# Performance work log

Hardware: AMD Instinct MI355X
Metric: run time of the kernel (lower is better)

Reference implementation:

```python
import jax, jax.numpy as jnp
import numpy as np

D, H, O, E, TOPK = 1024, 4096, 1024, 8, 2
B, L = 2, 2048
ROUTE_SCALE = 1.0


def setup_inputs() -> dict:
    key = jax.random.key(0)
    ks = jax.random.split(key, 7)
    # xavier-uniform bound for gate weight (E, D)
    gb = float(np.sqrt(6.0 / (E + D)))
    return {
        "x": jax.random.normal(ks[0], (B, L, D), dtype=jnp.float32),
        "gate_w": jax.random.uniform(ks[1], (E, D), jnp.float32, -gb, gb),
        "gate_b": jnp.zeros((E,), jnp.float32),
        "w1": jax.random.normal(ks[2], (E, D, H), jnp.float32) * 0.02,
        "b1": jnp.zeros((E, H), jnp.float32),
        "w2": jax.random.normal(ks[3], (E, H, O), jnp.float32) * 0.02,
        "b2": jnp.zeros((E, O), jnp.float32),
    }


def reference(x, gate_w, gate_b, w1, b1, w2, b2):
    Bb, Ll, Dd = x.shape
    N = Bb * Ll
    x_flat = x.reshape(N, Dd)  # (N, D)

    # ---- Gate: softmax router + top-k ----
    logits = x_flat @ gate_w.T + gate_b              # (N, E)
    probs = jax.nn.softmax(logits * ROUTE_SCALE, axis=-1)
    topk_vals, topk_idx = jax.lax.top_k(probs, TOPK)  # (N, K)

    # dense gate: zeros except selected experts keep their prob
    dense_gate = jnp.zeros((N, E), probs.dtype).at[
        jnp.arange(N)[:, None], topk_idx
    ].set(topk_vals)                                  # (N, E)

    # ---- Experts (vectorized over E; gate weights are exactly zero for
    #      non-selected experts, so the combine reproduces the sparse
    #      gather-MLP-scatter math of the original loop) ----
    h = jax.nn.relu(jnp.einsum("nd,edh->neh", x_flat, w1) + b1)  # (N, E, H)
    y = jnp.einsum("neh,eho->neo", h, w2) + b2                   # (N, E, O)
    out_flat = jnp.einsum("ne,neo->no", dense_gate, y)           # (N, O)

    return out_flat.reshape(Bb, Ll, O)
```

## Files before the change

### kernel.cpp

```cpp
#include <hip/hip_runtime.h>
#include <hip/hip_bf16.h>
#include <stdint.h>

#define NTOK 4096
#define DDIM 1024
#define HDIM 4096
#define ODIM 1024
#define NEXP 8
#define BM 128
#define BN 128
#define BK 64
#define CAPROWS (NTOK * 2 + NEXP * BM)
#define MAXTILES (CAPROWS / BM)

typedef float f32x4_t __attribute__((ext_vector_type(4)));
typedef short bf16x8_t __attribute__((ext_vector_type(8)));
using bf16_t = __hip_bfloat16;

__device__ __forceinline__ void gll16(const void* g, void* l) {
  __builtin_amdgcn_global_load_lds(
      (__attribute__((address_space(1))) void*)(void*)g,
      (__attribute__((address_space(3))) void*)l, 16, 0, 0);
}

__global__ __launch_bounds__(256) void gate_kernel(
    const float* __restrict__ x, const float* __restrict__ gw,
    const float* __restrict__ gb, int* __restrict__ top_idx,
    float* __restrict__ top_val, int* __restrict__ counts) {
  int n = blockIdx.x * 4 + (threadIdx.x >> 6);
  int l = threadIdx.x & 63;
  const float4* xv = (const float4*)(x + (size_t)n * DDIM);
  float4 xs[4];
#pragma unroll
  for (int j = 0; j < 4; ++j) xs[j] = xv[l + 64 * j];
  float part[NEXP];
#pragma unroll
  for (int e = 0; e < NEXP; ++e) {
    const float4* wv = (const float4*)(gw + (size_t)e * DDIM);
    float s = 0.f;
#pragma unroll
    for (int j = 0; j < 4; ++j) {
      float4 w4 = wv[l + 64 * j];
      s += xs[j].x * w4.x + xs[j].y * w4.y + xs[j].z * w4.z + xs[j].w * w4.w;
    }
    part[e] = s;
  }
#pragma unroll
  for (int off = 32; off > 0; off >>= 1)
#pragma unroll
    for (int e = 0; e < NEXP; ++e) part[e] += __shfl_xor(part[e], off, 64);

  float m = -1e30f;
#pragma unroll
  for (int e = 0; e < NEXP; ++e) { part[e] += gb[e]; m = fmaxf(m, part[e]); }
  float ssum = 0.f;
#pragma unroll
  for (int e = 0; e < NEXP; ++e) { part[e] = expf(part[e] - m); ssum += part[e]; }
  int i0 = 0; float v0 = part[0];
#pragma unroll
  for (int e = 1; e < NEXP; ++e) if (part[e] > v0) { v0 = part[e]; i0 = e; }
  int i1 = -1; float v1 = -1e30f;
#pragma unroll
  for (int e = 0; e < NEXP; ++e) if (e != i0 && part[e] > v1) { v1 = part[e]; i1 = e; }
  if (l == 0) {
    float inv = 1.f / ssum;
    top_idx[n * 2] = i0; top_idx[n * 2 + 1] = i1;
    top_val[n * 2] = v0 * inv; top_val[n * 2 + 1] = v1 * inv;
    atomicAdd(&counts[i0], 1); atomicAdd(&counts[i1], 1);
  }
}

__global__ void plan_kernel(const int* __restrict__ counts, int* __restrict__ offs,
                            int* __restrict__ tile_e, int* __restrict__ tile_r) {
  if (threadIdx.x != 0 || blockIdx.x != 0) return;
  int off = 0, t = 0;
  for (int e = 0; e < NEXP; ++e) {
    offs[e] = off;
    int padded = ((counts[e] + BM - 1) / BM) * BM;
    for (int r = 0; r < padded; r += BM) { tile_e[t] = e; tile_r[t] = off + r; ++t; }
    off += padded;
  }
  offs[NEXP] = off;
  for (; t < MAXTILES; ++t) { tile_e[t] = -1; tile_r[t] = 0; }
}

__global__ __launch_bounds__(128) void gather_kernel(
    const float* __restrict__ x, const int* __restrict__ top_idx,
    const int* __restrict__ offs, int* __restrict__ cursors,
    int* __restrict__ slot_for, bf16_t* __restrict__ Xg) {
  int a = blockIdx.x;
  __shared__ int s_slot;
  if (threadIdx.x == 0) {
    int e = top_idx[a];
    int pos = atomicAdd(&cursors[e], 1);
    int slot = offs[e] + pos;
    slot_for[a] = slot;
    s_slot = slot;
  }
  __syncthreads();
  int slot = s_slot;
  int n = a >> 1;
  const float4* xv = (const float4*)(x + (size_t)n * DDIM);
  float4 a0 = xv[threadIdx.x * 2], a1 = xv[threadIdx.x * 2 + 1];
  __align__(16) bf16_t tmp[8] = {
      __float2bfloat16(a0.x), __float2bfloat16(a0.y),
      __float2bfloat16(a0.z), __float2bfloat16(a0.w),
      __float2bfloat16(a1.x), __float2bfloat16(a1.y),
      __float2bfloat16(a1.z), __float2bfloat16(a1.w)};
  *(uint4*)(Xg + (size_t)slot * DDIM + threadIdx.x * 8) = *(const uint4*)tmp;
}

__global__ __launch_bounds__(256) void convT_kernel(
    const float* __restrict__ src, bf16_t* __restrict__ dst, int R, int C) {
  __shared__ float tile[64][65];
  int e = blockIdx.z;
  int c0 = blockIdx.x * 64, r0 = blockIdx.y * 64;
  const float* s = src + ((size_t)e * R + r0) * C + c0;
  int tc = threadIdx.x & 63, tr = threadIdx.x >> 6;
#pragma unroll
  for (int p = 0; p < 16; ++p) {
    int r = tr + p * 4;
    tile[r][tc] = s[(size_t)r * C + tc];
  }
  __syncthreads();
  bf16_t* d = dst + ((size_t)e * C + c0) * R + r0;
  int oc = threadIdx.x >> 2;
  int orq = (threadIdx.x & 3) * 16;
#pragma unroll
  for (int j = 0; j < 4; ++j) {
    __align__(8) bf16_t v[4];
#pragma unroll
    for (int i = 0; i < 4; ++i) v[i] = __float2bfloat16(tile[orq + j * 4 + i][oc]);
    *(uint2*)(d + (size_t)oc * R + orq + j * 4) = *(const uint2*)v;
  }
}

template <int KTOT, int NTOT, int WHICH>
__global__ __launch_bounds__(256, 2) void gemm_kernel(
    const bf16_t* __restrict__ A, const bf16_t* __restrict__ Bt,
    const float* __restrict__ bias, void* __restrict__ Cout,
    const int* __restrict__ tile_e, const int* __restrict__ tile_r) {
  int e = tile_e[blockIdx.y];
  if (e < 0) return;
  int row0 = tile_r[blockIdx.y];
  int n0 = blockIdx.x * BN;
  int tid = threadIdx.x;

  __shared__ bf16_t As[2][BM * BK];
  __shared__ bf16_t Bs[2][BN * BK];

  const bf16_t* Ab = A + (size_t)row0 * KTOT;
  const bf16_t* Bb = Bt + ((size_t)e * NTOT + n0) * KTOT;

  int l = tid & 63;
  int w = tid >> 6;
  int wr = (w >> 1) * 64;
  int wc = (w & 1) * 64;
  int lrow = l & 15, lk = l >> 4;

  int st_row = tid >> 3;
  int st_lc = (tid & 7) ^ (st_row & 7);

  int aoff[2][4], boff[2][4];
#pragma unroll
  for (int ks = 0; ks < 2; ++ks) {
    int pc = (ks * 4 + lk) ^ (l & 7);
#pragma unroll
    for (int f = 0; f < 4; ++f) {
      aoff[ks][f] = ((wr + f * 16 + lrow) * BK) * 2 + pc * 16;
      boff[ks][f] = ((wc + f * 16 + lrow) * BK) * 2 + pc * 16;
    }
  }

  f32x4_t acc[4][4];
#pragma unroll
  for (int i = 0; i < 4; ++i)
#pragma unroll
    for (int j = 0; j < 4; ++j) acc[i][j] = (f32x4_t){0.f, 0.f, 0.f, 0.f};

  const int NKT = KTOT / BK;

#pragma unroll
  for (int it = 0; it < 4; ++it) {
    int r = st_row + it * 32;
    gll16(Ab + (size_t)r * KTOT + st_lc * 8, (char*)As[0] + (it * 256 + tid) * 16);
    gll16(Bb + (size_t)r * KTOT + st_lc * 8, (char*)Bs[0] + (it * 256 + tid) * 16);
  }
  __syncthreads();

  int cur = 0;
  for (int kt = 0; kt < NKT; ++kt) {
    if (kt + 1 < NKT) {
      int kb = (kt + 1) * BK + st_lc * 8;
#pragma unroll
      for (int it = 0; it < 4; ++it) {
        int r = st_row + it * 32;
        gll16(Ab + (size_t)r * KTOT + kb, (char*)As[cur ^ 1] + (it * 256 + tid) * 16);
        gll16(Bb + (size_t)r * KTOT + kb, (char*)Bs[cur ^ 1] + (it * 256 + tid) * 16);
      }
    }
#pragma unroll
    for (int ks = 0; ks < 2; ++ks) {
      bf16x8_t av[4], bv[4];
#pragma unroll
      for (int f = 0; f < 4; ++f)
        av[f] = *(const bf16x8_t*)((const char*)As[cur] + aoff[ks][f]);
#pragma unroll
      for (int f = 0; f < 4; ++f)
        bv[f] = *(const bf16x8_t*)((const char*)Bs[cur] + boff[ks][f]);
#pragma unroll
      for (int fm = 0; fm < 4; ++fm)
#pragma unroll
        for (int fn = 0; fn < 4; ++fn)
          acc[fm][fn] = __builtin_amdgcn_mfma_f32_16x16x32_bf16(
              av[fm], bv[fn], acc[fm][fn], 0, 0, 0);
    }
    __syncthreads();
    cur ^= 1;
  }

#pragma unroll
  for (int fn = 0; fn < 4; ++fn) {
    int col = n0 + wc + fn * 16 + lrow;
    float bv = bias[e * NTOT + col];
#pragma unroll
    for (int fm = 0; fm < 4; ++fm) {
      size_t rbase = (size_t)row0 + wr + fm * 16 + lk * 4;
#pragma unroll
      for (int i = 0; i < 4; ++i) {
        float v = acc[fm][fn][i] + bv;
        if (WHICH == 1) {
          v = v > 0.f ? v : 0.f;
          ((bf16_t*)Cout)[(rbase + i) * NTOT + col] = __float2bfloat16(v);
        } else {
          ((float*)Cout)[(rbase + i) * NTOT + col] = v;
        }
      }
    }
  }
}

__global__ __launch_bounds__(256) void combine_kernel(
    const float* __restrict__ Y, const int* __restrict__ slot_for,
    const float* __restrict__ top_val, float* __restrict__ out) {
  int n = blockIdx.x;
  int s0 = slot_for[n * 2], s1 = slot_for[n * 2 + 1];
  float v0 = top_val[n * 2], v1 = top_val[n * 2 + 1];
  int t = threadIdx.x;
  float4 a = ((const float4*)(Y + (size_t)s0 * ODIM))[t];
  float4 b = ((const float4*)(Y + (size_t)s1 * ODIM))[t];
  float4 r;
  r.x = v0 * a.x + v1 * b.x;
  r.y = v0 * a.y + v1 * b.y;
  r.z = v0 * a.z + v1 * b.z;
  r.w = v0 * a.w + v1 * b.w;
  ((float4*)(out + (size_t)n * ODIM))[t] = r;
}

__global__ void zero_meta_kernel(int* p) {
  if (threadIdx.x < 16) p[threadIdx.x] = 0;
}

extern "C" void kernel_launch(void* const* d_in, const int* in_sizes, int n_in,
                              void* d_out, int out_size, void* d_ws, size_t ws_size,
                              hipStream_t stream) {
  const float* x  = (const float*)d_in[0];
  const float* gw = (const float*)d_in[1];
  const float* gb = (const float*)d_in[2];
  const float* w1 = (const float*)d_in[3];
  const float* b1 = (const float*)d_in[4];
  const float* w2 = (const float*)d_in[5];
  const float* b2 = (const float*)d_in[6];
  float* out = (float*)d_out;

  char* ws = (char*)d_ws;
  size_t off = 0;
  auto alloc = [&](size_t bytes) {
    void* p = ws + off;
    off = (off + bytes + 255) & ~(size_t)255;
    return p;
  };
  bf16_t* w1T = (bf16_t*)alloc((size_t)NEXP * HDIM * DDIM * 2);
  bf16_t* w2T = (bf16_t*)alloc((size_t)NEXP * ODIM * HDIM * 2);
  bf16_t* Xg  = (bf16_t*)alloc((size_t)CAPROWS * DDIM * 2);
  bf16_t* Hb  = (bf16_t*)alloc((size_t)CAPROWS * HDIM * 2);
  int* counts  = (int*)alloc(64);
  int* cursors = counts + 8;
  int* offs    = (int*)alloc(64);
  int* tile_e  = (int*)alloc(MAXTILES * 4);
  int* tile_r  = (int*)alloc(MAXTILES * 4);
  int* top_idx = (int*)alloc((size_t)NTOK * 2 * 4);
  float* top_val = (float*)alloc((size_t)NTOK * 2 * 4);
  int* slot_for = (int*)alloc((size_t)NTOK * 2 * 4);
  float* Yb = (float*)w1T;

  hipLaunchKernelGGL(zero_meta_kernel, dim3(1), dim3(64), 0, stream, counts);
  hipMemsetAsync(Xg, 0, (size_t)CAPROWS * DDIM * 2, stream);
  hipLaunchKernelGGL(convT_kernel, dim3(HDIM / 64, DDIM / 64, NEXP), dim3(256), 0,
                     stream, w1, w1T, DDIM, HDIM);
  hipLaunchKernelGGL(convT_kernel, dim3(ODIM / 64, HDIM / 64, NEXP), dim3(256), 0,
                     stream, w2, w2T, HDIM, ODIM);
  hipLaunchKernelGGL(gate_kernel, dim3(NTOK / 4), dim3(256), 0, stream,
                     x, gw, gb, top_idx, top_val, counts);
  hipLaunchKernelGGL(plan_kernel, dim3(1), dim3(1), 0, stream,
                     counts, offs, tile_e, tile_r);
  hipLaunchKernelGGL(gather_kernel, dim3(NTOK * 2), dim3(128), 0, stream,
                     x, top_idx, offs, cursors, slot_for, Xg);
  hipLaunchKernelGGL((gemm_kernel<DDIM, HDIM, 1>), dim3(HDIM / BN, MAXTILES),
                     dim3(256), 0, stream, Xg, w1T, b1, Hb, tile_e, tile_r);
  hipLaunchKernelGGL((gemm_kernel<HDIM, ODIM, 2>), dim3(ODIM / BN, MAXTILES),
                     dim3(256), 0, stream, Hb, w2T, b2, Yb, tile_e, tile_r);
  hipLaunchKernelGGL(combine_kernel, dim3(NTOK), dim3(256), 0, stream,
                     Yb, slot_for, top_val, out);
}
```

Before: 797.9 us.

## Replace expert GEMM with 256x256 8-wave pipelined kernel and XCD-aware tile swizzle

Rewrites the grouped expert GEMM to use 256x256 tiles with 8 waves, splitting the A and B loads into half-tile stages that overlap explicitly with MFMA phases. Explicit barriers, waitcnts and setprio control the schedule, and block ids are remapped so neighbouring tiles land on the same XCD. The transpose-convert kernel also switches to 16-byte stores. The larger tile raises data reuse and arithmetic intensity, but it also increases padding waste per expert (BM capacity grows) and lowers the block count, and it uses 128 KB of LDS per block.

Result: faster. 736.2 us (-7.7%).

```diff
diff --git a/kernel.cpp b/kernel.cpp
--- a/kernel.cpp
+++ b/kernel.cpp
@@ -7,8 +7,8 @@
 #define HDIM 4096
 #define ODIM 1024
 #define NEXP 8
-#define BM 128
-#define BN 128
+#define BM 256
+#define BN 256
 #define BK 64
 #define CAPROWS (NTOK * 2 + NEXP * BM)
 #define MAXTILES (CAPROWS / BM)
@@ -16,6 +16,23 @@
 typedef float f32x4_t __attribute__((ext_vector_type(4)));
 typedef short bf16x8_t __attribute__((ext_vector_type(8)));
 using bf16_t = __hip_bfloat16;
+
+#define S_BARRIER()                         \
+  do {                                      \
+    __builtin_amdgcn_sched_barrier(0);      \
+    __builtin_amdgcn_s_barrier();           \
+    __builtin_amdgcn_sched_barrier(0);      \
+  } while (0)
+#define WAIT_LGKM0()                                  \
+  do {                                                \
+    asm volatile("s_waitcnt lgkmcnt(0)" ::: "memory");\
+    __builtin_amdgcn_sched_barrier(0);                \
+  } while (0)
+#define WAIT_VMCNT(n)                                       \
+  do {                                                      \
+    asm volatile("s_waitcnt vmcnt(" #n ")" ::: "memory");   \
+    __builtin_amdgcn_sched_barrier(0);                      \
+  } while (0)
 
 __device__ __forceinline__ void gll16(const void* g, void* l) {
   __builtin_amdgcn_global_load_lds(
@@ -123,117 +140,164 @@
     tile[r][tc] = s[(size_t)r * C + tc];
   }
   __syncthreads();
-  bf16_t* d = dst + ((size_t)e * C + c0) * R + r0;
-  int oc = threadIdx.x >> 2;
-  int orq = (threadIdx.x & 3) * 16;
-#pragma unroll
-  for (int j = 0; j < 4; ++j) {
-    __align__(8) bf16_t v[4];
-#pragma unroll
-    for (int i = 0; i < 4; ++i) v[i] = __float2bfloat16(tile[orq + j * 4 + i][oc]);
-    *(uint2*)(d + (size_t)oc * R + orq + j * 4) = *(const uint2*)v;
+  bf16_t* dcol = dst + ((size_t)e * C + c0) * R + r0;
+  int t = threadIdx.x;
+#pragma unroll
+  for (int it = 0; it < 2; ++it) {
+    int c = (t >> 3) + it * 32;
+    int r8 = (t & 7) * 8;
+    __align__(16) bf16_t v[8];
+#pragma unroll
+    for (int j = 0; j < 8; ++j) v[j] = __float2bfloat16(tile[r8 + j][c]);
+    *(uint4*)(dcol + (size_t)c * R + r8) = *(const uint4*)v;
   }
 }
 
 template <int KTOT, int NTOT, int WHICH>
-__global__ __launch_bounds__(256, 2) void gemm_kernel(
+__global__ __launch_bounds__(512, 2) void gemm8_kernel(
     const bf16_t* __restrict__ A, const bf16_t* __restrict__ Bt,
     const float* __restrict__ bias, void* __restrict__ Cout,
     const int* __restrict__ tile_e, const int* __restrict__ tile_r) {
-  int e = tile_e[blockIdx.y];
+  constexpr int NCOL = NTOT / BN;
+  int nwg = gridDim.x;
+  int bid = blockIdx.x;
+  int q = nwg >> 3, rr = nwg & 7;
+  int xcd = bid & 7, pos = bid >> 3;
+  int swz = (xcd < rr ? xcd * (q + 1) : rr * (q + 1) + (xcd - rr) * q) + pos;
+  int ty = swz / NCOL, tx = swz % NCOL;
+
+  int e = tile_e[ty];
   if (e < 0) return;
-  int row0 = tile_r[blockIdx.y];
-  int n0 = blockIdx.x * BN;
+  int row0 = tile_r[ty];
+  int n0 = tx * BN;
+
+  __shared__ char smem[131072];
   int tid = threadIdx.x;
-
-  __shared__ bf16_t As[2][BM * BK];
-  __shared__ bf16_t Bs[2][BN * BK];
+  int w = tid >> 6, l = tid & 63;
+  int wm = w >> 2, wn = w & 3;
+  int lrow = l & 15, lk = l >> 4;
 
   const bf16_t* Ab = A + (size_t)row0 * KTOT;
   const bf16_t* Bb = Bt + ((size_t)e * NTOT + n0) * KTOT;
 
-  int l = tid & 63;
-  int w = tid >> 6;
-  int wr = (w >> 1) * 64;
-  int wc = (w & 1) * 64;
-  int lrow = l & 15, lk = l >> 4;
-
-  int st_row = tid >> 3;
-  int st_lc = (tid & 7) ^ (st_row & 7);
-
-  int aoff[2][4], boff[2][4];
-#pragma unroll
-  for (int ks = 0; ks < 2; ++ks) {
-    int pc = (ks * 4 + lk) ^ (l & 7);
-#pragma unroll
-    for (int f = 0; f < 4; ++f) {
-      aoff[ks][f] = ((wr + f * 16 + lrow) * BK) * 2 + pc * 16;
-      boff[ks][f] = ((wc + f * 16 + lrow) * BK) * 2 + pc * 16;
+  int sidx0 = tid, sidx1 = 512 + tid;
+  int sr0 = sidx0 >> 3, sc0 = (sidx0 & 7) ^ (sr0 & 7);
+  int sr1 = sidx1 >> 3, sc1 = (sidx1 & 7) ^ (sr1 & 7);
+
+  auto stageA = [&](int kt, int h, int d) {
+    char* lb = smem + d * 32768 + h * 16384;
+    const bf16_t* g = Ab + (size_t)(h * 128) * KTOT + kt * BK;
+    gll16(g + (size_t)sr0 * KTOT + sc0 * 8, lb + sidx0 * 16);
+    gll16(g + (size_t)sr1 * KTOT + sc1 * 8, lb + sidx1 * 16);
+  };
+  auto stageB = [&](int kt, int h, int d) {
+    char* lb = smem + 65536 + d * 32768 + h * 16384;
+    const bf16_t* g = Bb + (size_t)(h * 128) * KTOT + kt * BK;
+    gll16(g + (size_t)sr0 * KTOT + sc0 * 8, lb + sidx0 * 16);
+    gll16(g + (size_t)sr1 * KTOT + sc1 * 8, lb + sidx1 * 16);
+  };
+
+  int abase = (wm * 128 + lrow) * 128;
+  int bbase = (wn * 64 + lrow) * 128;
+  int p0 = ((lk) ^ (lrow & 7)) * 16;
+  int p1 = ((4 + lk) ^ (lrow & 7)) * 16;
+
+  f32x4_t acc[8][4];
+#pragma unroll
+  for (int m = 0; m < 8; ++m)
+#pragma unroll
+    for (int n = 0; n < 4; ++n) acc[m][n] = (f32x4_t){0.f, 0.f, 0.f, 0.f};
+
+  const int NKT = KTOT / BK;
+
+  stageA(0, 0, 0); stageA(0, 1, 0);
+  stageB(0, 0, 0); stageB(0, 1, 0);
+  stageA(1, 0, 1); stageA(1, 1, 1);
+  WAIT_VMCNT(4);
+  S_BARRIER();
+
+  for (int t = 0; t < NKT; ++t) {
+    int d = t & 1;
+    const char* Ad = smem + d * 32768;
+    const char* Bd = smem + 65536 + d * 32768;
+    bf16x8_t ak0[8], ak1[8], bv[4];
+#pragma unroll
+    for (int m = 0; m < 8; ++m)
+      ak0[m] = *(const bf16x8_t*)(Ad + abase + m * 2048 + p0);
+#pragma unroll
+    for (int n = 0; n < 4; ++n)
+      bv[n] = *(const bf16x8_t*)(Bd + bbase + n * 2048 + p0);
+    if (t + 1 < NKT) stageB(t + 1, 0, d ^ 1);
+    S_BARRIER();
+    WAIT_LGKM0();
+    __builtin_amdgcn_s_setprio(1);
+#pragma unroll
+    for (int m = 0; m < 4; ++m)
+#pragma unroll
+      for (int n = 0; n < 4; ++n)
+        acc[m][n] = __builtin_amdgcn_mfma_f32_16x16x32_bf16(ak0[m], bv[n], acc[m][n], 0, 0, 0);
+    __builtin_amdgcn_s_setprio(0);
+    S_BARRIER();
+#pragma unroll
+    for (int m = 0; m < 8; ++m)
+      ak1[m] = *(const bf16x8_t*)(Ad + abase + m * 2048 + p1);
+    if (t + 1 < NKT) stageB(t + 1, 1, d ^ 1);
+    S_BARRIER();
+    WAIT_LGKM0();
+    __builtin_amdgcn_s_setprio(1);
+#pragma unroll
+    for (int m = 4; m < 8; ++m)
+#pragma unroll
+      for (int n = 0; n < 4; ++n)
+        acc[m][n] = __builtin_amdgcn_mfma_f32_16x16x32_bf16(ak0[m], bv[n], acc[m][n], 0, 0, 0);
+    __builtin_amdgcn_s_setprio(0);
+    S_BARRIER();
+#pragma unroll
+    for (int n = 0; n < 4; ++n)
+      bv[n] = *(const bf16x8_t*)(Bd + bbase + n * 2048 + p1);
+    if (t + 2 < NKT) stageA(t + 2, 0, d);
+    S_BARRIER();
+    WAIT_LGKM0();
+    __builtin_amdgcn_s_setprio(1);
+#pragma unroll
+    for (int m = 0; m < 4; ++m)
+#pragma unroll
+      for (int n = 0; n < 4; ++n)
+        acc[m][n] = __builtin_amdgcn_mfma_f32_16x16x32_bf16(ak1[m], bv[n], acc[m][n], 0, 0, 0);
+    __builtin_amdgcn_s_setprio(0);
+    S_BARRIER();
+    if (t + 2 < NKT) {
+      stageA(t + 2, 1, d);
+      WAIT_VMCNT(4);
+    } else {
+      WAIT_VMCNT(0);
     }
-  }
-
-  f32x4_t acc[4][4];
-#pragma unroll
-  for (int i = 0; i < 4; ++i)
-#pragma unroll
-    for (int j = 0; j < 4; ++j) acc[i][j] = (f32x4_t){0.f, 0.f, 0.f, 0.f};
-
-  const int NKT = KTOT / BK;
-
-#pragma unroll
-  for (int it = 0; it < 4; ++it) {
-    int r = st_row + it * 32;
-    gll16(Ab + (size_t)r * KTOT + st_lc * 8, (char*)As[0] + (it * 256 + tid) * 16);
-    gll16(Bb + (size_t)r * KTOT + st_lc * 8, (char*)Bs[0] + (it * 256 + tid) * 16);
-  }
-  __syncthreads();
-
-  int cur = 0;
-  for (int kt = 0; kt < NKT; ++kt) {
-    if (kt + 1 < NKT) {
-      int kb = (kt + 1) * BK + st_lc * 8;
-#pragma unroll
-      for (int it = 0; it < 4; ++it) {
-        int r = st_row + it * 32;
-        gll16(Ab + (size_t)r * KTOT + kb, (char*)As[cur ^ 1] + (it * 256 + tid) * 16);
-        gll16(Bb + (size_t)r * KTOT + kb, (char*)Bs[cur ^ 1] + (it * 256 + tid) * 16);
-      }
-    }
-#pragma unroll
-    for (int ks = 0; ks < 2; ++ks) {
-      bf16x8_t av[4], bv[4];
-#pragma unroll
-      for (int f = 0; f < 4; ++f)
-        av[f] = *(const bf16x8_t*)((const char*)As[cur] + aoff[ks][f]);
-#pragma unroll
-      for (int f = 0; f < 4; ++f)
-        bv[f] = *(const bf16x8_t*)((const char*)Bs[cur] + boff[ks][f]);
-#pragma unroll
-      for (int fm = 0; fm < 4; ++fm)
-#pragma unroll
-        for (int fn = 0; fn < 4; ++fn)
-          acc[fm][fn] = __builtin_amdgcn_mfma_f32_16x16x32_bf16(
-              av[fm], bv[fn], acc[fm][fn], 0, 0, 0);
-    }
-    __syncthreads();
-    cur ^= 1;
-  }
-
-#pragma unroll
-  for (int fn = 0; fn < 4; ++fn) {
-    int col = n0 + wc + fn * 16 + lrow;
-    float bv = bias[e * NTOT + col];
-#pragma unroll
-    for (int fm = 0; fm < 4; ++fm) {
-      size_t rbase = (size_t)row0 + wr + fm * 16 + lk * 4;
+    S_BARRIER();
+    __builtin_amdgcn_s_setprio(1);
+#pragma unroll
+    for (int m = 4; m < 8; ++m)
+#pragma unroll
+      for (int n = 0; n < 4; ++n)
+        acc[m][n] = __builtin_amdgcn_mfma_f32_16x16x32_bf16(ak1[m], bv[n], acc[m][n], 0, 0, 0);
+    __builtin_amdgcn_s_setprio(0);
+    S_BARRIER();
+  }
+
+#pragma unroll
+  for (int n = 0; n < 4; ++n) {
+    int col = n0 + wn * 64 + n * 16 + lrow;
+    float bb = bias[e * NTOT + col];
+#pragma unroll
+    for (int m = 0; m < 8; ++m) {
+      size_t rb = (size_t)row0 + wm * 128 + m * 16 + lk * 4;
 #pragma unroll
       for (int i = 0; i < 4; ++i) {
-        float v = acc[fm][fn][i] + bv;
+        float v = acc[m][n][i] + bb;
         if (WHICH == 1) {
           v = v > 0.f ? v : 0.f;
-          ((bf16_t*)Cout)[(rbase + i) * NTOT + col] = __float2bfloat16(v);
+          ((bf16_t*)Cout)[(rb + i) * NTOT + col] = __float2bfloat16(v);
         } else {
-          ((float*)Cout)[(rbase + i) * NTOT + col] = v;
+          ((float*)Cout)[(rb + i) * NTOT + col] = v;
         }
       }
     }
@@ -306,10 +370,12 @@
                      counts, offs, tile_e, tile_r);
   hipLaunchKernelGGL(gather_kernel, dim3(NTOK * 2), dim3(128), 0, stream,
                      x, top_idx, offs, cursors, slot_for, Xg);
-  hipLaunchKernelGGL((gemm_kernel<DDIM, HDIM, 1>), dim3(HDIM / BN, MAXTILES),
-                     dim3(256), 0, stream, Xg, w1T, b1, Hb, tile_e, tile_r);
-  hipLaunchKernelGGL((gemm_kernel<HDIM, ODIM, 2>), dim3(ODIM / BN, MAXTILES),
-                     dim3(256), 0, stream, Hb, w2T, b2, Yb, tile_e, tile_r);
+  hipLaunchKernelGGL((gemm8_kernel<DDIM, HDIM, 1>),
+                     dim3((HDIM / BN) * MAXTILES), dim3(512), 0, stream,
+                     Xg, w1T, b1, Hb, tile_e, tile_r);
+  hipLaunchKernelGGL((gemm8_kernel<HDIM, ODIM, 2>),
+                     dim3((ODIM / BN) * MAXTILES), dim3(512), 0, stream,
+                     Hb, w2T, b2, Yb, tile_e, tile_r);
   hipLaunchKernelGGL(combine_kernel, dim3(NTOK), dim3(256), 0, stream,
                      Yb, slot_for, top_val, out);
 }
```
